# Kernel optimization log

Hardware: AMD Instinct MI355X
Metric: run time of the kernel (lower is better)

## Reference

```python
import jax, jax.numpy as jnp
import numpy as np

B, T, C, H = 2, 2048, 2048, 16
HD = C // H  # head dim = 128


def setup_inputs() -> dict:
    key = jax.random.key(0)
    k1, k2, k3 = jax.random.split(key, 3)
    x = jax.random.normal(k1, (B, T, C), dtype=jnp.float32)
    # torch Linear stores weight as [out_features, in_features]; y = x @ W.T
    w_attn = jax.random.normal(k2, (3 * C, C), dtype=jnp.float32) * (C ** -0.5)
    w_proj = jax.random.normal(k3, (C, C), dtype=jnp.float32) * (C ** -0.5)
    b_proj = jnp.zeros((C,), dtype=jnp.float32)
    return {"x": x, "w_attn": w_attn, "w_proj": w_proj, "b_proj": b_proj}


def reference(x, w_attn, w_proj, b_proj):
    # c_attn: [B,T,C] -> [B,T,3C], then split into q,k,v
    qkv = jnp.einsum('btc,oc->bto', x, w_attn)
    q, k, v = jnp.split(qkv, 3, axis=-1)
    # [B,T,C] -> [B,H,T,HD]
    q = q.reshape(B, T, H, HD).transpose(0, 2, 1, 3)
    k = k.reshape(B, T, H, HD).transpose(0, 2, 1, 3)
    v = v.reshape(B, T, H, HD).transpose(0, 2, 1, 3)
    scale = 1.0 / jnp.sqrt(jnp.float32(HD))
    att = jnp.einsum('bhqd,bhkd->bhqk', q, k) * scale  # [B,H,T,T]
    causal = jnp.tril(jnp.ones((T, T), dtype=bool))
    att = jnp.where(causal, att, -jnp.inf)
    att = jax.nn.softmax(att, axis=-1)
    # dropout p=0.0 (eval): identity
    y = jnp.einsum('bhqk,bhkd->bhqd', att, v)  # [B,H,T,HD]
    y = y.transpose(0, 2, 1, 3).reshape(B, T, C)
    y = jnp.einsum('btc,oc->bto', y, w_proj) + b_proj
    return y
```

## Files before the change

kernel.cpp:

```cpp
#include <hip/hip_runtime.h>
#include <hip/hip_bf16.h>
#include <stdint.h>
#include <stddef.h>

#define Bn  2
#define Tn  2048
#define Cn  2048
#define Hn  16
#define HDn 128

typedef short short8   __attribute__((ext_vector_type(8)));
typedef short short8_a __attribute__((ext_vector_type(8), may_alias));
typedef unsigned int u32x4_a __attribute__((ext_vector_type(4), may_alias));
typedef unsigned short u16x4_a __attribute__((ext_vector_type(4), may_alias));
typedef unsigned short u16x8_a __attribute__((ext_vector_type(8), may_alias));
typedef float f32x4 __attribute__((ext_vector_type(4)));

typedef __attribute__((address_space(1))) const void av1_t;
typedef __attribute__((address_space(3))) void av3_t;

__device__ inline unsigned short f2b(float f) {
    union { float f; unsigned u; } v; v.f = f;
    unsigned r = v.u + 0x7fffu + ((v.u >> 16) & 1u);
    return (unsigned short)(r >> 16);
}
__device__ inline u16x4_a cvt4_f32_bf16(u32x4_a v) {
    u16x4_a h;
#pragma unroll
    for (int e = 0; e < 4; e++) {
        unsigned u = v[e];
        unsigned r = u + 0x7fffu + ((u >> 16) & 1u);
        h[e] = (unsigned short)(r >> 16);
    }
    return h;
}

__global__ __launch_bounds__(256)
void cvt_kernel(const float* __restrict__ src, unsigned short* __restrict__ dst, int n)
{
    const int i = (blockIdx.x * 256 + threadIdx.x) * 8;
    if (i >= n) return;
    u32x4_a a = *(const u32x4_a*)((const unsigned*)src + i);
    u32x4_a b = *(const u32x4_a*)((const unsigned*)src + i + 4);
    u16x8_a o;
    u16x4_a ha = cvt4_f32_bf16(a), hb = cvt4_f32_bf16(b);
#pragma unroll
    for (int e = 0; e < 4; e++) { o[e] = ha[e]; o[e + 4] = hb[e]; }
    *(u16x8_a*)(dst + i) = o;
}

template<int OUT_F32, int HAS_BIAS>
__global__ __launch_bounds__(256)
void gemm_bb_kernel(const unsigned short* __restrict__ A,
                    const unsigned short* __restrict__ Bm,
                    const float* __restrict__ bias, void* __restrict__ Cv,
                    int M, int N, int K)
{
    __shared__ __align__(16) unsigned short As[128 * 32];
    __shared__ __align__(16) unsigned short Bs[128 * 32];

    const int tid  = threadIdx.x;
    const int lane = tid & 63;
    const int wave = tid >> 6;
    const int quad = lane >> 4;
    const int l15  = lane & 15;
    const int tm = blockIdx.x * 128;
    const int tn = blockIdx.y * 128;
    const int wr = (wave >> 1) * 64;
    const int wc = (wave & 1) * 64;

    const int srow = lane >> 2;
    const int scol = (lane & 3) * 8;

    f32x4 acc[4][4];
#pragma unroll
    for (int i = 0; i < 4; i++)
#pragma unroll
        for (int j = 0; j < 4; j++) acc[i][j] = (f32x4){0.f, 0.f, 0.f, 0.f};

    const int ksteps = K >> 5;
    for (int kt = 0; kt < ksteps; ++kt) {
        const int k0 = kt << 5;
#pragma unroll
        for (int r = 0; r < 2; r++) {
            const int row = (r * 4 + wave) * 16 + srow;
            __builtin_amdgcn_global_load_lds(
                (av1_t*)(A + (size_t)(tm + row) * K + k0 + scol),
                (av3_t*)(&As[row * 32 + scol]), 16, 0, 0);
            __builtin_amdgcn_global_load_lds(
                (av1_t*)(Bm + (size_t)(tn + row) * K + k0 + scol),
                (av3_t*)(&Bs[row * 32 + scol]), 16, 0, 0);
        }
        asm volatile("s_waitcnt vmcnt(0)" ::: "memory");
        __syncthreads();

        short8 af[4], bf[4];
#pragma unroll
        for (int i = 0; i < 4; i++)
            af[i] = (short8)(*(const short8_a*)&As[(wr + i * 16 + l15) * 32 + quad * 8]);
#pragma unroll
        for (int j = 0; j < 4; j++)
            bf[j] = (short8)(*(const short8_a*)&Bs[(wc + j * 16 + l15) * 32 + quad * 8]);
#pragma unroll
        for (int i = 0; i < 4; i++)
#pragma unroll
            for (int j = 0; j < 4; j++)
                acc[i][j] = __builtin_amdgcn_mfma_f32_16x16x32_bf16(af[i], bf[j], acc[i][j], 0, 0, 0);
        __syncthreads();
    }

#pragma unroll
    for (int i = 0; i < 4; i++) {
        const int row = tm + wr + i * 16 + quad * 4;
#pragma unroll
        for (int j = 0; j < 4; j++) {
            const int col = tn + wc + j * 16 + l15;
            const float bv = HAS_BIAS ? bias[col] : 0.0f;
#pragma unroll
            for (int r = 0; r < 4; r++) {
                if (OUT_F32)
                    ((float*)Cv)[(size_t)(row + r) * N + col] = acc[i][j][r] + bv;
                else
                    ((unsigned short*)Cv)[(size_t)(row + r) * N + col] = f2b(acc[i][j][r] + bv);
            }
        }
    }
}

#define LA0 0
#define LB0 16384
#define LA1 32768
#define LB1 49152

template<int NBM, int NBN, int MODE>
__global__ __launch_bounds__(512, 2)
void gemm8_kernel(const unsigned short* __restrict__ A,
                  const unsigned short* __restrict__ Bm,
                  const float* __restrict__ bias,
                  unsigned short* __restrict__ qout,
                  unsigned short* __restrict__ kvout,
                  float* __restrict__ fout)
{
    __shared__ __align__(16) unsigned short lds[65536];

    const int tid  = threadIdx.x;
    const int lane = tid & 63;
    const int wave = tid >> 6;
    const int quad = lane >> 4;
    const int l15  = lane & 15;
    const int wrow = wave >> 2;
    const int wcol = wave & 3;
    const int swz  = (l15 & 7) << 3;

    const int bid  = blockIdx.x;
    const int xcd  = bid & 7;
    const int sl   = bid >> 3;
    const int tile = xcd * (NBM * NBN / 8) + sl;
    const int bm   = tile % NBM;
    const int bn   = tile / NBM;
    const int tm   = bm * 256;
    const int tn   = bn * 256;

    const unsigned short* Ab = A  + (size_t)tm * Cn;
    const unsigned short* Bb = Bm + (size_t)tn * Cn;

    f32x4 acc[8][4];
#pragma unroll
    for (int i = 0; i < 8; i++)
#pragma unroll
        for (int j = 0; j < 4; j++) acc[i][j] = (f32x4){0.f, 0.f, 0.f, 0.f};

    auto stage = [&](const unsigned short* g, int kt, int base, int half) {
#pragma unroll
        for (int rr = 0; rr < 2; ++rr) {
            const int idx = rr * 512 + tid;
            const int row = idx >> 3;
            const int ks  = ((idx & 7) * 8) ^ ((row & 7) << 3);
            __builtin_amdgcn_global_load_lds(
                (av1_t*)(g + (size_t)(half * 128 + row) * Cn + kt * 64 + ks),
                (av3_t*)(lds + base + half * 8192 + idx * 8), 16, 0, 0);
        }
    };
    auto lda = [&](int base, int i, int ks) -> short8 {
        return (short8)(*(const short8_a*)&lds[base + (wrow * 128 + i * 16 + l15) * 64
                                               + ((ks * 32 + quad * 8) ^ swz)]);
    };
    auto ldb = [&](int base, int j, int ks) -> short8 {
        return (short8)(*(const short8_a*)&lds[base + (wcol * 64 + j * 16 + l15) * 64
                                               + ((ks * 32 + quad * 8) ^ swz)]);
    };

    stage(Ab, 0, LA0, 0); stage(Ab, 0, LA0, 1);
    stage(Bb, 0, LB0, 0); stage(Bb, 0, LB0, 1);
    stage(Ab, 1, LA1, 0); stage(Ab, 1, LA1, 1);
    asm volatile("s_waitcnt vmcnt(4)" ::: "memory");
    __builtin_amdgcn_s_barrier();

    const int nt = Cn / 64;
    for (int t = 0; t < nt; t += 2) {
        const bool tail = (t + 2 >= nt);
        short8 af[8][2], bf[2][2];

#pragma unroll
        for (int i = 0; i < 4; i++) { af[i][0] = lda(LA0, i, 0); af[i][1] = lda(LA0, i, 1); }
#pragma unroll
        for (int j = 0; j < 2; j++) { bf[j][0] = ldb(LB0, j, 0); bf[j][1] = ldb(LB0, j, 1); }
        stage(Bb, t + 1, LB1, 0);
        __builtin_amdgcn_s_barrier();
        asm volatile("s_waitcnt lgkmcnt(0)" ::: "memory");
        __builtin_amdgcn_s_setprio(1);
#pragma unroll
        for (int ks = 0; ks < 2; ks++)
#pragma unroll
            for (int i = 0; i < 4; i++)
#pragma unroll
                for (int j = 0; j < 2; j++)
                    acc[i][j] = __builtin_amdgcn_mfma_f32_16x16x32_bf16(af[i][ks], bf[j][ks], acc[i][j], 0, 0, 0);
        __builtin_amdgcn_s_setprio(0);
        __builtin_amdgcn_s_barrier();

#pragma unroll
        for (int i = 4; i < 8; i++) { af[i][0] = lda(LA0, i, 0); af[i][1] = lda(LA0, i, 1); }
        stage(Bb, t + 1, LB1, 1);
        __builtin_amdgcn_s_barrier();
        asm volatile("s_waitcnt lgkmcnt(0)" ::: "memory");
        __builtin_amdgcn_s_setprio(1);
#pragma unroll
        for (int ks = 0; ks < 2; ks++)
#pragma unroll
            for (int i = 4; i < 8; i++)
#pragma unroll
                for (int j = 0; j < 2; j++)
                    acc[i][j] = __builtin_amdgcn_mfma_f32_16x16x32_bf16(af[i][ks], bf[j][ks], acc[i][j], 0, 0, 0);
        __builtin_amdgcn_s_setprio(0);
        __builtin_amdgcn_s_barrier();

#pragma unroll
        for (int j = 0; j < 2; j++) { bf[j][0] = ldb(LB0, 2 + j, 0); bf[j][1] = ldb(LB0, 2 + j, 1); }
        if (!tail) stage(Ab, t + 2, LA0, 0);
        __builtin_amdgcn_s_barrier();
        asm volatile("s_waitcnt lgkmcnt(0)" ::: "memory");
        __builtin_amdgcn_s_setprio(1);
#pragma unroll
        for (int ks = 0; ks < 2; ks++)
#pragma unroll
            for (int i = 0; i < 4; i++)
#pragma unroll
                for (int j = 0; j < 2; j++)
                    acc[i][2 + j] = __builtin_amdgcn_mfma_f32_16x16x32_bf16(af[i][ks], bf[j][ks], acc[i][2 + j], 0, 0, 0);
        __builtin_amdgcn_s_setprio(0);
        __builtin_amdgcn_s_barrier();

        if (!tail) stage(Ab, t + 2, LA0, 1);
        __builtin_amdgcn_s_barrier();
        __builtin_amdgcn_s_setprio(1);
#pragma unroll
        for (int ks = 0; ks < 2; ks++)
#pragma unroll
            for (int i = 4; i < 8; i++)
#pragma unroll
                for (int j = 0; j < 2; j++)
                    acc[i][2 + j] = __builtin_amdgcn_mfma_f32_16x16x32_bf16(af[i][ks], bf[j][ks], acc[i][2 + j], 0, 0, 0);
        __builtin_amdgcn_s_setprio(0);
        if (tail) asm volatile("s_waitcnt vmcnt(0)" ::: "memory");
        else      asm volatile("s_waitcnt vmcnt(4)" ::: "memory");
        __builtin_amdgcn_s_barrier();

#pragma unroll
        for (int i = 0; i < 4; i++) { af[i][0] = lda(LA1, i, 0); af[i][1] = lda(LA1, i, 1); }
#pragma unroll
        for (int j = 0; j < 2; j++) { bf[j][0] = ldb(LB1, j, 0); bf[j][1] = ldb(LB1, j, 1); }
        if (!tail) stage(Bb, t + 2, LB0, 0);
        __builtin_amdgcn_s_barrier();
        asm volatile("s_waitcnt lgkmcnt(0)" ::: "memory");
        __builtin_amdgcn_s_setprio(1);
#pragma unroll
        for (int ks = 0; ks < 2; ks++)
#pragma unroll
            for (int i = 0; i < 4; i++)
#pragma unroll
                for (int j = 0; j < 2; j++)
                    acc[i][j] = __builtin_amdgcn_mfma_f32_16x16x32_bf16(af[i][ks], bf[j][ks], acc[i][j], 0, 0, 0);
        __builtin_amdgcn_s_setprio(0);
        __builtin_amdgcn_s_barrier();

#pragma unroll
        for (int i = 4; i < 8; i++) { af[i][0] = lda(LA1, i, 0); af[i][1] = lda(LA1, i, 1); }
        if (!tail) stage(Bb, t + 2, LB0, 1);
        __builtin_amdgcn_s_barrier();
        asm volatile("s_waitcnt lgkmcnt(0)" ::: "memory");
        __builtin_amdgcn_s_setprio(1);
#pragma unroll
        for (int ks = 0; ks < 2; ks++)
#pragma unroll
            for (int i = 4; i < 8; i++)
#pragma unroll
                for (int j = 0; j < 2; j++)
                    acc[i][j] = __builtin_amdgcn_mfma_f32_16x16x32_bf16(af[i][ks], bf[j][ks], acc[i][j], 0, 0, 0);
        __builtin_amdgcn_s_setprio(0);
        __builtin_amdgcn_s_barrier();

#pragma unroll
        for (int j = 0; j < 2; j++) { bf[j][0] = ldb(LB1, 2 + j, 0); bf[j][1] = ldb(LB1, 2 + j, 1); }
        if (!tail) stage(Ab, t + 3, LA1, 0);
        __builtin_amdgcn_s_barrier();
        asm volatile("s_waitcnt lgkmcnt(0)" ::: "memory");
        __builtin_amdgcn_s_setprio(1);
#pragma unroll
        for (int ks = 0; ks < 2; ks++)
#pragma unroll
            for (int i = 0; i < 4; i++)
#pragma unroll
                for (int j = 0; j < 2; j++)
                    acc[i][2 + j] = __builtin_amdgcn_mfma_f32_16x16x32_bf16(af[i][ks], bf[j][ks], acc[i][2 + j], 0, 0, 0);
        __builtin_amdgcn_s_setprio(0);
        __builtin_amdgcn_s_barrier();

        if (!tail) stage(Ab, t + 3, LA1, 1);
        __builtin_amdgcn_s_barrier();
        __builtin_amdgcn_s_setprio(1);
#pragma unroll
        for (int ks = 0; ks < 2; ks++)
#pragma unroll
            for (int i = 4; i < 8; i++)
#pragma unroll
                for (int j = 0; j < 2; j++)
                    acc[i][2 + j] = __builtin_amdgcn_mfma_f32_16x16x32_bf16(af[i][ks], bf[j][ks], acc[i][2 + j], 0, 0, 0);
        __builtin_amdgcn_s_setprio(0);
        if (tail) asm volatile("s_waitcnt vmcnt(0)" ::: "memory");
        else      asm volatile("s_waitcnt vmcnt(4)" ::: "memory");
        __builtin_amdgcn_s_barrier();
    }

    if (MODE == 0) {
        unsigned short* obase = (tn < Cn) ? qout : kvout;
        const int cofs    = (tn < Cn) ? 0 : Cn;
        const size_t ostr = (tn < Cn) ? Cn : 2 * Cn;
#pragma unroll
        for (int i = 0; i < 8; i++) {
            const int row = tm + wrow * 128 + i * 16 + quad * 4;
#pragma unroll
            for (int j = 0; j < 4; j++) {
                const int col = tn + wcol * 64 + j * 16 + l15 - cofs;
#pragma unroll
                for (int r = 0; r < 4; r++)
                    obase[(size_t)(row + r) * ostr + col] = f2b(acc[i][j][r]);
            }
        }
    } else {
        const int Nn = NBN * 256;
#pragma unroll
        for (int i = 0; i < 8; i++) {
            const int row = tm + wrow * 128 + i * 16 + quad * 4;
#pragma unroll
            for (int j = 0; j < 4; j++) {
                const int col = tn + wcol * 64 + j * 16 + l15;
                const float bv = bias[col];
#pragma unroll
                for (int r = 0; r < 4; r++)
                    fout[(size_t)(row + r) * Nn + col] = acc[i][j][r] + bv;
            }
        }
    }
}

__global__ __launch_bounds__(512, 2)
void attn_kernel(const unsigned short* __restrict__ q,
                 const unsigned short* __restrict__ kv,
                 unsigned short* __restrict__ outp)
{
    __shared__ __align__(16) unsigned short Ks[128 * 136];
    __shared__ __align__(16) unsigned short Vs[128 * 136];
    __shared__ __align__(16) unsigned short Ps[8][16 * 136];

    const int qp   = blockIdx.x;
    const int bh   = blockIdx.y;
    const int b    = bh >> 4;
    const int h    = bh & 15;
    const int tid  = threadIdx.x;
    const int lane = tid & 63;
    const int wave = tid >> 6;
    const int quad = lane >> 4;
    const int l15  = lane & 15;

    short8 ones;
#pragma unroll
    for (int e = 0; e < 8; e++) ones[e] = (short)0x3F80;

    for (int half = 0; half < 2; ++half) {
        const int qt = half ? (15 - qp) : qp;
        const int qrow0 = qt * 128 + wave * 16;

        short8 qf[4];
#pragma unroll
        for (int kk = 0; kk < 4; kk++) {
            const unsigned short* p = q + (size_t)(b * Tn + qrow0 + l15) * Cn
                                      + h * HDn + kk * 32 + quad * 8;
            qf[kk] = (short8)(*(const short8_a*)p);
        }

        float m_i[4], l_i[4];
        f32x4 o_acc[8];
#pragma unroll
        for (int r = 0; r < 4; r++) { m_i[r] = -1e30f; l_i[r] = 0.f; }
#pragma unroll
        for (int jd = 0; jd < 8; jd++) o_acc[jd] = (f32x4){0.f, 0.f, 0.f, 0.f};

        const int ktiles = qt + 1;

        u32x4_a kr[4], vr[4];
        auto preload = [&](int kt2) {
            const int kk0 = kt2 * 128;
#pragma unroll
            for (int rep = 0; rep < 4; ++rep) {
                const int idx  = tid + rep * 512;
                const int krow = idx >> 4;
                const int dg   = (idx & 15) * 8;
                const size_t rb = (size_t)(b * Tn + kk0 + krow) * (2 * Cn) + h * HDn + dg;
                kr[rep] = *(const u32x4_a*)(kv + rb);
                vr[rep] = *(const u32x4_a*)(kv + rb + Cn);
            }
        };
        preload(0);

        for (int kt2 = 0; kt2 < ktiles; ++kt2) {
            const int kk0 = kt2 * 128;
            __syncthreads();
#pragma unroll
            for (int rep = 0; rep < 4; ++rep) {
                const int idx  = tid + rep * 512;
                const int krow = idx >> 4;
                const int l    = idx & 15;
                const int dg   = l * 8;
                *(u32x4_a*)&Ks[krow * 136 + dg] = kr[rep];
                const int pcol = krow ^ ((l & 7) << 3);
                const unsigned short* ve = (const unsigned short*)&vr[rep];
#pragma unroll
                for (int e = 0; e < 8; e++) Vs[(dg + e) * 136 + pcol] = ve[e];
            }
            __syncthreads();
            if (kt2 + 1 < ktiles) preload(kt2 + 1);

            f32x4 s[8];
#pragma unroll
            for (int j = 0; j < 8; j++) s[j] = (f32x4){0.f, 0.f, 0.f, 0.f};
            __builtin_amdgcn_s_setprio(1);
#pragma unroll
            for (int kk = 0; kk < 4; ++kk) {
                short8 kf[8];
#pragma unroll
                for (int j = 0; j < 8; j++)
                    kf[j] = (short8)(*(const short8_a*)&Ks[(j * 16 + l15) * 136 + kk * 32 + quad * 8]);
#pragma unroll
                for (int j = 0; j < 8; j++)
                    s[j] = __builtin_amdgcn_mfma_f32_16x16x32_bf16(qf[kk], kf[j], s[j], 0, 0, 0);
            }
            __builtin_amdgcn_s_setprio(0);

            const bool needmask = (kk0 + 127 > qrow0);
            float alr[4];
#pragma unroll
            for (int r = 0; r < 4; r++) {
                const int qidx = qrow0 + quad * 4 + r;
                float mx = -1e30f;
#pragma unroll
                for (int j = 0; j < 8; j++) {
                    float v = s[j][r] * 0.08838834764831845f;
                    if (needmask) {
                        const int kidx = kk0 + j * 16 + l15;
                        v = (kidx <= qidx) ? v : -1e30f;
                    }
                    s[j][r] = v;
                    mx = fmaxf(mx, v);
                }
#pragma unroll
                for (int off = 1; off < 16; off <<= 1)
                    mx = fmaxf(mx, __shfl_xor(mx, off));
                const float mn = fmaxf(m_i[r], mx);
                alr[r] = __expf(fminf(m_i[r] - mn, 0.f));
                m_i[r] = mn;
#pragma unroll
                for (int j = 0; j < 8; j++) {
                    const float p = __expf(fminf(s[j][r] - mn, 0.f));
                    s[j][r] = p;
                }
#pragma unroll
                for (int jd = 0; jd < 8; jd++) o_acc[jd][r] *= alr[r];
#pragma unroll
                for (int j = 0; j < 8; j++)
                    Ps[wave][(quad * 4 + r) * 136 + j * 16 + l15] = f2b(s[j][r]);
            }
            asm volatile("s_waitcnt lgkmcnt(0)" ::: "memory");

            f32x4 lacc = (f32x4){0.f, 0.f, 0.f, 0.f};
            __builtin_amdgcn_s_setprio(1);
#pragma unroll
            for (int kk2 = 0; kk2 < 4; ++kk2) {
                short8 pf = (short8)(*(const short8_a*)&Ps[wave][l15 * 136 + kk2 * 32 + quad * 8]);
#pragma unroll
                for (int jd = 0; jd < 8; jd++) {
                    const int d = jd * 16 + l15;
                    const int g = (d >> 3) & 7;
                    const int colb = ((4 * kk2 + quad) ^ g) * 8;
                    short8 vf = (short8)(*(const short8_a*)&Vs[d * 136 + colb]);
                    o_acc[jd] = __builtin_amdgcn_mfma_f32_16x16x32_bf16(pf, vf, o_acc[jd], 0, 0, 0);
                }
                lacc = __builtin_amdgcn_mfma_f32_16x16x32_bf16(pf, ones, lacc, 0, 0, 0);
            }
            __builtin_amdgcn_s_setprio(0);
#pragma unroll
            for (int r = 0; r < 4; r++)
                l_i[r] = l_i[r] * alr[r] + lacc[r];
        }

#pragma unroll
        for (int r = 0; r < 4; r++) {
            const float inv = 1.0f / fmaxf(l_i[r], 1e-20f);
            const int trow = qrow0 + quad * 4 + r;
#pragma unroll
            for (int jd = 0; jd < 8; jd++) {
                const int col = h * HDn + jd * 16 + l15;
                outp[(size_t)(b * Tn + trow) * Cn + col] = f2b(o_acc[jd][r] * inv);
            }
        }
    }
}

extern "C" void kernel_launch(void* const* d_in, const int* in_sizes, int n_in,
                              void* d_out, int out_size, void* d_ws, size_t ws_size,
                              hipStream_t stream)
{
    const float* x      = (const float*)d_in[0];
    const float* w_attn = (const float*)d_in[1];
    const float* w_proj = (const float*)d_in[2];
    const float* b_proj = (const float*)d_in[3];
    float* out = (float*)d_out;

    const size_t MiB = 1024 * 1024;
    unsigned short* kvbuf = (unsigned short*)d_out;

    const int nx   = Bn * Tn * Cn;
    const int nwq  = Cn * Cn;
    const int nwkv = 2 * Cn * Cn;

    if (ws_size >= 56 * MiB) {
        unsigned short* xb   = (unsigned short*)d_ws;
        unsigned short* qbuf = (unsigned short*)((char*)d_ws + 16 * MiB);
        unsigned short* wb   = (unsigned short*)((char*)d_ws + 32 * MiB);
        const int nwa = 3 * Cn * Cn;

        cvt_kernel<<<nx / 8 / 256, 256, 0, stream>>>(x, xb, nx);
        cvt_kernel<<<nwa / 8 / 256, 256, 0, stream>>>(w_attn, wb, nwa);
        gemm8_kernel<16, 16, 0><<<dim3(256), 512, 0, stream>>>(xb, wb, nullptr,
                                                               qbuf, kvbuf, nullptr);
        gemm_bb_kernel<0, 0><<<dim3(32, 16), 256, 0, stream>>>(
            xb, wb + (size_t)2 * Cn * Cn, nullptr, kvbuf + Cn,
            Bn * Tn, 2 * Cn, Cn);
        attn_kernel<<<dim3(8, Bn * Hn), 512, 0, stream>>>(qbuf, kvbuf, qbuf);
        cvt_kernel<<<nwq / 8 / 256, 256, 0, stream>>>(w_proj, wb, nwq);
        gemm_bb_kernel<1, 1><<<dim3(32, 16), 256, 0, stream>>>(qbuf, wb, b_proj, out,
                                                               Bn * Tn, Cn, Cn);
    } else {
        unsigned short* xb   = (unsigned short*)d_ws;
        unsigned short* qbuf = (unsigned short*)((char*)d_ws + 16 * MiB);
        unsigned short* wb   = (unsigned short*)((char*)d_ws + 32 * MiB);

        cvt_kernel<<<nx / 8 / 256, 256, 0, stream>>>(x, xb, nx);
        cvt_kernel<<<nwq / 8 / 256, 256, 0, stream>>>(w_attn, wb, nwq);
        gemm_bb_kernel<0, 0><<<dim3(32, 16), 256, 0, stream>>>(xb, wb, nullptr, qbuf,
                                                               Bn * Tn, Cn, Cn);
        cvt_kernel<<<nwkv / 8 / 256, 256, 0, stream>>>(w_attn + (size_t)Cn * Cn, wb, nwkv);
        gemm_bb_kernel<0, 0><<<dim3(32, 32), 256, 0, stream>>>(xb, wb, nullptr, kvbuf,
                                                               Bn * Tn, 2 * Cn, Cn);
        attn_kernel<<<dim3(8, Bn * Hn), 512, 0, stream>>>(qbuf, kvbuf, qbuf);
        cvt_kernel<<<nwq / 8 / 256, 256, 0, stream>>>(w_proj, wb, nwq);
        gemm_bb_kernel<1, 1><<<dim3(32, 16), 256, 0, stream>>>(qbuf, wb, b_proj, out,
                                                               Bn * Tn, Cn, Cn);
    }
}
```

Measured before the change: 389.9 us.

## Merge input conversions, pad P tile stride, remap attention grid to 1D

Three separate tweaks. The x and w_attn fp32-to-bf16 conversions become one combined launch, removing a kernel launch. The per-wave P scratch stride in LDS changes from 136 to 140 to alter the bank-conflict pattern on P writes and reads. The attention grid becomes a flat 1D launch with a custom block-to-(head, q-pair) mapping, intended to spread heads across XCDs or CUs differently for cache locality. The new stride uses slightly more LDS.

```diff
diff --git a/kernel.cpp b/kernel.cpp
--- a/kernel.cpp
+++ b/kernel.cpp
@@ -8,6 +8,7 @@
 #define Cn  2048
 #define Hn  16
 #define HDn 128
+#define PSTR 140
 
 typedef short short8   __attribute__((ext_vector_type(8)));
 typedef short short8_a __attribute__((ext_vector_type(8), may_alias));
@@ -35,11 +36,9 @@
     return h;
 }
 
-__global__ __launch_bounds__(256)
-void cvt_kernel(const float* __restrict__ src, unsigned short* __restrict__ dst, int n)
-{
-    const int i = (blockIdx.x * 256 + threadIdx.x) * 8;
-    if (i >= n) return;
+__device__ inline void cvt_body(const float* __restrict__ src,
+                                unsigned short* __restrict__ dst, int i)
+{
     u32x4_a a = *(const u32x4_a*)((const unsigned*)src + i);
     u32x4_a b = *(const u32x4_a*)((const unsigned*)src + i + 4);
     u16x8_a o;
@@ -47,6 +46,24 @@
 #pragma unroll
     for (int e = 0; e < 4; e++) { o[e] = ha[e]; o[e + 4] = hb[e]; }
     *(u16x8_a*)(dst + i) = o;
+}
+
+__global__ __launch_bounds__(256)
+void cvt_kernel(const float* __restrict__ src, unsigned short* __restrict__ dst, int n)
+{
+    const int i = (blockIdx.x * 256 + threadIdx.x) * 8;
+    if (i >= n) return;
+    cvt_body(src, dst, i);
+}
+
+__global__ __launch_bounds__(256)
+void cvt2_kernel(const float* __restrict__ s0, unsigned short* __restrict__ d0, int n0,
+                 const float* __restrict__ s1, unsigned short* __restrict__ d1, int n1)
+{
+    int i = (blockIdx.x * 256 + threadIdx.x) * 8;
+    if (i < n0) { cvt_body(s0, d0, i); return; }
+    i -= n0;
+    if (i < n1) cvt_body(s1, d1, i);
 }
 
 template<int OUT_F32, int HAS_BIAS>
@@ -371,10 +388,11 @@
 {
     __shared__ __align__(16) unsigned short Ks[128 * 136];
     __shared__ __align__(16) unsigned short Vs[128 * 136];
-    __shared__ __align__(16) unsigned short Ps[8][16 * 136];
-
-    const int qp   = blockIdx.x;
-    const int bh   = blockIdx.y;
+    __shared__ __align__(16) unsigned short Ps[8][16 * PSTR];
+
+    const int bid  = blockIdx.x;
+    const int qp   = (bid >> 3) & 7;
+    const int bh   = (bid & 7) * 4 + (bid >> 6);
     const int b    = bh >> 4;
     const int h    = bh & 15;
     const int tid  = threadIdx.x;
@@ -488,7 +506,7 @@
                 for (int jd = 0; jd < 8; jd++) o_acc[jd][r] *= alr[r];
 #pragma unroll
                 for (int j = 0; j < 8; j++)
-                    Ps[wave][(quad * 4 + r) * 136 + j * 16 + l15] = f2b(s[j][r]);
+                    Ps[wave][(quad * 4 + r) * PSTR + j * 16 + l15] = f2b(s[j][r]);
             }
             asm volatile("s_waitcnt lgkmcnt(0)" ::: "memory");
 
@@ -496,7 +514,7 @@
             __builtin_amdgcn_s_setprio(1);
 #pragma unroll
             for (int kk2 = 0; kk2 < 4; ++kk2) {
-                short8 pf = (short8)(*(const short8_a*)&Ps[wave][l15 * 136 + kk2 * 32 + quad * 8]);
+                short8 pf = (short8)(*(const short8_a*)&Ps[wave][l15 * PSTR + kk2 * 32 + quad * 8]);
 #pragma unroll
                 for (int jd = 0; jd < 8; jd++) {
                     const int d = jd * 16 + l15;
@@ -549,14 +567,13 @@
         unsigned short* wb   = (unsigned short*)((char*)d_ws + 32 * MiB);
         const int nwa = 3 * Cn * Cn;
 
-        cvt_kernel<<<nx / 8 / 256, 256, 0, stream>>>(x, xb, nx);
-        cvt_kernel<<<nwa / 8 / 256, 256, 0, stream>>>(w_attn, wb, nwa);
+        cvt2_kernel<<<(nx + nwa) / 8 / 256, 256, 0, stream>>>(x, xb, nx, w_attn, wb, nwa);
         gemm8_kernel<16, 16, 0><<<dim3(256), 512, 0, stream>>>(xb, wb, nullptr,
                                                                qbuf, kvbuf, nullptr);
         gemm_bb_kernel<0, 0><<<dim3(32, 16), 256, 0, stream>>>(
             xb, wb + (size_t)2 * Cn * Cn, nullptr, kvbuf + Cn,
             Bn * Tn, 2 * Cn, Cn);
-        attn_kernel<<<dim3(8, Bn * Hn), 512, 0, stream>>>(qbuf, kvbuf, qbuf);
+        attn_kernel<<<dim3(256), 512, 0, stream>>>(qbuf, kvbuf, qbuf);
         cvt_kernel<<<nwq / 8 / 256, 256, 0, stream>>>(w_proj, wb, nwq);
         gemm_bb_kernel<1, 1><<<dim3(32, 16), 256, 0, stream>>>(qbuf, wb, b_proj, out,
                                                                Bn * Tn, Cn, Cn);
@@ -572,7 +589,7 @@
         cvt_kernel<<<nwkv / 8 / 256, 256, 0, stream>>>(w_attn + (size_t)Cn * Cn, wb, nwkv);
         gemm_bb_kernel<0, 0><<<dim3(32, 32), 256, 0, stream>>>(xb, wb, nullptr, kvbuf,
                                                                Bn * Tn, 2 * Cn, Cn);
-        attn_kernel<<<dim3(8, Bn * Hn), 512, 0, stream>>>(qbuf, kvbuf, qbuf);
+        attn_kernel<<<dim3(256), 512, 0, stream>>>(qbuf, kvbuf, qbuf);
         cvt_kernel<<<nwq / 8 / 256, 256, 0, stream>>>(w_proj, wb, nwq);
         gemm_bb_kernel<1, 1><<<dim3(32, 16), 256, 0, stream>>>(qbuf, wb, b_proj, out,
                                                                Bn * Tn, Cn, Cn);
```

Result: no change. 387.6 us (-0.6%).
